# Performance work log

Measured on AMD Instinct MI355X. Metric: run time of the kernel, lower is better.

The kernel has to match this reference:

```python
import jax, jax.numpy as jnp
import numpy as np

B, T, H = 256, 512, 256


def setup_inputs() -> dict:
    key = jax.random.key(0)
    ks = jax.random.split(key, 16)
    s_in, s_h = 1.0 / np.sqrt(1.0), 1.0 / np.sqrt(H)

    def u(k, shape, s):
        return jax.random.uniform(k, shape, jnp.float32, -s, s)

    return {
        "x": jax.random.normal(ks[0], (B, T), jnp.float32),
        # LSTMCell 1: input size 1
        "W_ih1": u(ks[1], (4 * H, 1), s_h), "b_ih1": u(ks[2], (4 * H,), s_h),
        "W_hh1": u(ks[3], (4 * H, H), s_h), "b_hh1": u(ks[4], (4 * H,), s_h),
        # LSTMCell 2: input size H
        "W_ih2": u(ks[5], (4 * H, H), s_h), "b_ih2": u(ks[6], (4 * H,), s_h),
        "W_hh2": u(ks[7], (4 * H, H), s_h), "b_hh2": u(ks[8], (4 * H,), s_h),
        # SelfAttention linears
        "Wa1": u(ks[9], (H, H), s_h), "ba1": u(ks[10], (H,), s_h),
        "Wa2": u(ks[11], (H, H), s_h), "ba2": u(ks[12], (H,), s_h),
        # output linear H -> 1
        "Wo": u(ks[13], (1, H), s_h), "bo": u(ks[14], (1,), s_h),
        "future": 0,
    }


def _lstm_cell(h, c, gates):
    i, f, g, o = jnp.split(gates, 4, axis=-1)
    i, f, o = jax.nn.sigmoid(i), jax.nn.sigmoid(f), jax.nn.sigmoid(o)
    g = jnp.tanh(g)
    c = f * c + i * g
    return o * jnp.tanh(c), c


def reference(x, W_ih1, b_ih1, W_hh1, b_hh1, W_ih2, b_ih2, W_hh2, b_hh2,
              Wa1, ba1, Wa2, ba2, Wo, bo, future):
    n, Tt = x.shape
    Hd = W_hh1.shape[1]

    def step_core(h1, c1, h2, c2, x_t):
        # x_t: [B, 1]
        g1 = x_t @ W_ih1.T + b_ih1 + h1 @ W_hh1.T + b_hh1
        h1, c1 = _lstm_cell(h1, c1, g1)
        g2 = h1 @ W_ih2.T + b_ih2 + h2 @ W_hh2.T + b_hh2
        h2, c2 = _lstm_cell(h2, c2, g2)
        # additive self-attention (dropout p=0 -> identity)
        attn = jax.nn.softmax(jnp.tanh(h2 @ Wa1.T + ba1) @ Wa2.T + ba2, axis=-1)
        out = (attn * h2) @ Wo.T + bo  # [B, 1]
        return h1, c1, h2, c2, out

    def step(carry, x_t):
        h1, c1, h2, c2, _ = carry
        h1, c1, h2, c2, out = step_core(h1, c1, h2, c2, x_t)
        return (h1, c1, h2, c2, out), out

    z = jnp.zeros((n, Hd), x.dtype)
    init = (z, z, z, z, jnp.zeros((n, 1), x.dtype))
    xs = x.T[:, :, None]  # [T, B, 1]
    carry, outs = jax.lax.scan(step, init, xs)

    if future > 0:
        def fstep(carry, _):
            h1, c1, h2, c2, out = carry
            h1, c1, h2, c2, out = step_core(h1, c1, h2, c2, out)
            return (h1, c1, h2, c2, out), out
        _, fouts = jax.lax.scan(fstep, carry, None, length=future)
        outs = jnp.concatenate([outs, fouts], axis=0)

    return outs[:, :, 0].T  # [B, T+future]
```

## Files before the change

kernel.cpp:

```cpp
#include <hip/hip_runtime.h>
#include <hip/hip_bf16.h>

#define HD   256
#define TT   512

typedef unsigned short u16;
typedef unsigned int   u32;
typedef unsigned long long u64;
typedef __attribute__((ext_vector_type(8))) short  short8;
typedef __attribute__((ext_vector_type(4))) float  f32x4;

__device__ __forceinline__ float bf2f(u16 v) { return __uint_as_float(((u32)v) << 16); }
__device__ __forceinline__ u16 f2bf(float f) {
    u32 u = __float_as_uint(f);
    u32 r = u + 0x7fffu + ((u >> 16) & 1u);
    return (u16)(r >> 16);
}
__device__ __forceinline__ float sigf(float x)  { return __builtin_amdgcn_rcpf(1.f + __expf(-x)); }
__device__ __forceinline__ float tanhf_(float x){ float e = __expf(-2.f * x);
                                                  return 2.f * __builtin_amdgcn_rcpf(1.f + e) - 1.f; }

__global__ void cvt_bf_kernel(const float* __restrict__ src, u16* __restrict__ dst, int n) {
    int idx = blockIdx.x * 256 + threadIdx.x;
    if (idx < n) dst[idx] = f2bf(src[idx]);
}

__global__ void bias_kernel(const float* __restrict__ a1, const float* __restrict__ b1,
                            const float* __restrict__ a2, const float* __restrict__ b2,
                            float* __restrict__ o1, float* __restrict__ o2) {
    int i = blockIdx.x * 256 + threadIdx.x;
    o1[i] = a1[i] + b1[i];
    o2[i] = a2[i] + b2[i];
}

__device__ __forceinline__ void load_bfrag(const float* __restrict__ W, int row, int kq, short8* bw) {
#pragma unroll
    for (int kk = 0; kk < 8; ++kk) {
        const float* p = W + row * 256 + kk * 32 + kq * 8;
        short8 s;
#pragma unroll
        for (int j = 0; j < 8; ++j) s[j] = (short)f2bf(p[j]);
        bw[kk] = s;
    }
}

__device__ __forceinline__ u64 aload64(const u64* p) {
    return __hip_atomic_load(p, __ATOMIC_RELAXED, __HIP_MEMORY_SCOPE_AGENT);
}
__device__ __forceinline__ void astore32(u32* p, u32 v) {
    __hip_atomic_store(p, v, __ATOMIC_RELAXED, __HIP_MEMORY_SCOPE_AGENT);
}

__device__ __forceinline__ void flag_wait(const u32* flags, int gb, u32 target) {
    if (threadIdx.x < 8) {
        const u32* slot = flags + (gb * 8 + (int)threadIdx.x) * 32;
        int sp = 0;
        while (__hip_atomic_load(slot, __ATOMIC_RELAXED, __HIP_MEMORY_SCOPE_AGENT) < target) {
            if (++sp > (1 << 24)) break;
        }
    }
    __syncthreads();
}

__device__ __forceinline__ void flag_post(u32* flags, int slotidx, u32 val) {
    __syncthreads();
    if (threadIdx.x == 0)
        __hip_atomic_store(flags + slotidx * 32, val, __ATOMIC_RELAXED, __HIP_MEMORY_SCOPE_AGENT);
}

__global__ __launch_bounds__(512) void lstm_persist(
    const float* __restrict__ x,
    const float* __restrict__ Wih1,
    const float* __restrict__ bias1,
    const float* __restrict__ bias2,
    const float* __restrict__ Whh1,
    const float* __restrict__ Wih2,
    const float* __restrict__ Whh2,
    u32* __restrict__ Hb1, u32* __restrict__ Hb2,
    u16* __restrict__ H2out, u32* flags)
{
    __shared__ __align__(16) u16 sh1hi[16 * 264], sh1lo[16 * 264];
    __shared__ __align__(16) u16 sh2hi[16 * 264], sh2lo[16 * 264];
    __shared__ float xs[TT * 16];
    __shared__ float gbuf1[4 * 16 * 36], gbuf2[4 * 16 * 36];
    __shared__ float wihs[128], b1s[128], b2s[128];

    const int tid = threadIdx.x;
    const int blk = blockIdx.x;
    const int gb = blk >> 3, hg = blk & 7;
    const int l = tid & 63, wv = tid >> 6;
    const int g = wv >> 1, hh = wv & 1;
    const int nloc = l & 15, kq = l >> 4;
    const int wrow = g * 256 + hg * 32 + hh * 16 + nloc;

    short8 bW1[8], bW2[8], bW3[8];
    load_bfrag(Whh1, wrow, kq, bW1);
    load_bfrag(Wih2, wrow, kq, bW2);
    load_bfrag(Whh2, wrow, kq, bW3);

    for (int idx = tid; idx < 16 * TT; idx += 512) {
        int b = idx >> 9, t = idx & 511;
        xs[t * 16 + b] = x[(gb * 16 + b) * TT + t];
    }
    if (tid < 128) {
        int rr = (tid >> 5) * 256 + hg * 32 + (tid & 31);
        wihs[tid] = Wih1[rr]; b1s[tid] = bias1[rr]; b2s[tid] = bias2[rr];
    }

    const int cb = tid >> 5, ci = tid & 31;
    const int bg = gb * 16 + cb, ig = hg * 32 + ci;
#pragma unroll
    for (int pp = 0; pp < 2; ++pp) {
        astore32(&Hb1[((pp * 256 + bg) << 8) + ig], 0u);
        astore32(&Hb2[((pp * 256 + bg) << 8) + ig], 0u);
    }
    float c1 = 0.f, c2 = 0.f;

    flag_post(flags, gb * 8 + hg, 1u);

    const int aoff = nloc * 264 + kq * 8;
    const int sb = tid >> 5, scol = (tid & 31) * 8;
    const int sbase = sb * 264 + scol;

    for (int k = 0; k <= TT; ++k) {
        flag_wait(flags, gb, (u32)(k + 1));

        const int rp = k & 1, wp = rp ^ 1;
        {
            const u32* p1 = Hb1 + ((rp * 256 + gb * 16 + sb) << 8) + scol;
            const u32* p2 = Hb2 + ((rp * 256 + gb * 16 + sb) << 8) + scol;
            u32 w1v[8], w2v[8];
#pragma unroll
            for (int j = 0; j < 4; ++j) {
                u64 t = aload64((const u64*)p1 + j);
                w1v[2 * j] = (u32)t; w1v[2 * j + 1] = (u32)(t >> 32);
            }
#pragma unroll
            for (int j = 0; j < 4; ++j) {
                u64 t = aload64((const u64*)p2 + j);
                w2v[2 * j] = (u32)t; w2v[2 * j + 1] = (u32)(t >> 32);
            }
            u32 h1h[4], h1l[4], h2h[4], h2l[4];
#pragma unroll
            for (int i = 0; i < 4; ++i) {
                u32 a = w1v[2 * i], b = w1v[2 * i + 1];
                h1h[i] = (a & 0xffffu) | (b << 16);
                h1l[i] = (a >> 16) | (b & 0xffff0000u);
                a = w2v[2 * i]; b = w2v[2 * i + 1];
                h2h[i] = (a & 0xffffu) | (b << 16);
                h2l[i] = (a >> 16) | (b & 0xffff0000u);
            }
            *(uint4*)(sh1hi + sbase) = *(uint4*)(h1h);
            *(uint4*)(sh1lo + sbase) = *(uint4*)(h1l);
            *(uint4*)(sh2hi + sbase) = *(uint4*)(h2h);
            *(uint4*)(sh2lo + sbase) = *(uint4*)(h2l);
        }
        __syncthreads();

        f32x4 acc1a = {0,0,0,0}, acc1b = {0,0,0,0};
        f32x4 acc2a = {0,0,0,0}, acc2b = {0,0,0,0};
#pragma unroll
        for (int kk = 0; kk < 8; ++kk) {
            short8 a1h = *(const short8*)(sh1hi + aoff + kk * 32);
            short8 a1l = *(const short8*)(sh1lo + aoff + kk * 32);
            if (k < TT) {
                acc1a = __builtin_amdgcn_mfma_f32_16x16x32_bf16(a1h, bW1[kk], acc1a, 0, 0, 0);
                acc1b = __builtin_amdgcn_mfma_f32_16x16x32_bf16(a1l, bW1[kk], acc1b, 0, 0, 0);
            }
            if (k > 0) {
                acc2a = __builtin_amdgcn_mfma_f32_16x16x32_bf16(a1h, bW2[kk], acc2a, 0, 0, 0);
                acc2b = __builtin_amdgcn_mfma_f32_16x16x32_bf16(a1l, bW2[kk], acc2b, 0, 0, 0);
                short8 a2h = *(const short8*)(sh2hi + aoff + kk * 32);
                short8 a2l = *(const short8*)(sh2lo + aoff + kk * 32);
                acc2a = __builtin_amdgcn_mfma_f32_16x16x32_bf16(a2h, bW3[kk], acc2a, 0, 0, 0);
                acc2b = __builtin_amdgcn_mfma_f32_16x16x32_bf16(a2l, bW3[kk], acc2b, 0, 0, 0);
            }
        }
#pragma unroll
        for (int r = 0; r < 4; ++r) {
            int m = (l >> 4) * 4 + r;
            gbuf1[(g * 16 + m) * 36 + hh * 16 + nloc] = acc1a[r] + acc1b[r];
            gbuf2[(g * 16 + m) * 36 + hh * 16 + nloc] = acc2a[r] + acc2b[r];
        }
        __syncthreads();

        u16 hi2 = 0;
        if (k < TT) {
            float xv = xs[k * 16 + cb];
            float g0 = gbuf1[(0 * 16 + cb) * 36 + ci] + xv * wihs[ci]      + b1s[ci];
            float g1 = gbuf1[(1 * 16 + cb) * 36 + ci] + xv * wihs[32 + ci] + b1s[32 + ci];
            float g2 = gbuf1[(2 * 16 + cb) * 36 + ci] + xv * wihs[64 + ci] + b1s[64 + ci];
            float g3 = gbuf1[(3 * 16 + cb) * 36 + ci] + xv * wihs[96 + ci] + b1s[96 + ci];
            float ii = sigf(g0), ff = sigf(g1), gg = tanhf_(g2), oo = sigf(g3);
            c1 = ff * c1 + ii * gg;
            float h = oo * tanhf_(c1);
            u16 hi = f2bf(h); u32 word = (u32)hi | ((u32)f2bf(h - bf2f(hi)) << 16);
            astore32(&Hb1[((wp * 256 + bg) << 8) + ig], word);
        }
        if (k > 0) {
            float g0 = gbuf2[(0 * 16 + cb) * 36 + ci] + b2s[ci];
            float g1 = gbuf2[(1 * 16 + cb) * 36 + ci] + b2s[32 + ci];
            float g2 = gbuf2[(2 * 16 + cb) * 36 + ci] + b2s[64 + ci];
            float g3 = gbuf2[(3 * 16 + cb) * 36 + ci] + b2s[96 + ci];
            float ii = sigf(g0), ff = sigf(g1), gg = tanhf_(g2), oo = sigf(g3);
            c2 = ff * c2 + ii * gg;
            float h = oo * tanhf_(c2);
            hi2 = f2bf(h); u32 word = (u32)hi2 | ((u32)f2bf(h - bf2f(hi2)) << 16);
            astore32(&Hb2[((wp * 256 + bg) << 8) + ig], word);
        }
        flag_post(flags, gb * 8 + hg, (u32)(k + 2));
        if (k > 0) H2out[(bg * TT + (k - 1)) * 256 + ig] = hi2;
    }
}

__global__ __launch_bounds__(256) void attn_fused(
    const u16*  __restrict__ Wa1b, const u16* __restrict__ Wa2b,
    const float* __restrict__ ba1, const float* __restrict__ ba2,
    const float* __restrict__ Wo,  const float* __restrict__ bo,
    const u16*  __restrict__ H2,   float* __restrict__ out)
{
    __shared__ __align__(16) u16 sA[64 * 264];
    __shared__ __align__(16) u16 sP[64 * 264];
    __shared__ float red[64 * 12];
    __shared__ float sb1[256], sb2[256], swo[256];

    const int tid = threadIdx.x;
    const int w = tid >> 6, l = tid & 63;
    const int c = l & 15, q = l >> 4;
    const int row0 = blockIdx.x * 64;

    {
        const int r = tid >> 2, qq = tid & 3;
        const uint4* src = (const uint4*)(H2 + (row0 + r) * 256 + qq * 64);
#pragma unroll
        for (int j = 0; j < 8; ++j) {
            uint4 v = src[j];
            *(uint4*)(sA + r * 264 + qq * 64 + j * 8) = v;
        }
    }
    if (tid < 256) { sb1[tid] = ba1[tid]; sb2[tid] = ba2[tid]; swo[tid] = Wo[tid]; }
    __syncthreads();

    f32x4 acc[4][4];
#pragma unroll
    for (int mi = 0; mi < 4; ++mi)
#pragma unroll
        for (int ni = 0; ni < 4; ++ni) acc[mi][ni] = (f32x4){0,0,0,0};

#pragma unroll
    for (int ni = 0; ni < 4; ++ni) {
        const int row = w * 64 + ni * 16 + c;
        const u16* wp = Wa1b + row * 256 + q * 8;
        short8 bW[8];
#pragma unroll
        for (int kk = 0; kk < 8; ++kk) bW[kk] = *(const short8*)(wp + kk * 32);
#pragma unroll
        for (int kk = 0; kk < 8; ++kk)
#pragma unroll
            for (int mi = 0; mi < 4; ++mi) {
                short8 a = *(const short8*)(sA + (mi * 16 + c) * 264 + q * 8 + kk * 32);
                acc[mi][ni] = __builtin_amdgcn_mfma_f32_16x16x32_bf16(a, bW[kk], acc[mi][ni], 0, 0, 0);
            }
    }
#pragma unroll
    for (int mi = 0; mi < 4; ++mi)
#pragma unroll
        for (int ni = 0; ni < 4; ++ni) {
            const int n = w * 64 + ni * 16 + c;
            const float bj = sb1[n];
#pragma unroll
            for (int r = 0; r < 4; ++r) {
                int m = mi * 16 + q * 4 + r;
                sP[m * 264 + n] = f2bf(tanhf(acc[mi][ni][r] + bj));
            }
        }
    __syncthreads();

#pragma unroll
    for (int mi = 0; mi < 4; ++mi)
#pragma unroll
        for (int ni = 0; ni < 4; ++ni) acc[mi][ni] = (f32x4){0,0,0,0};
#pragma unroll
    for (int ni = 0; ni < 4; ++ni) {
        const int row = w * 64 + ni * 16 + c;
        const u16* wp = Wa2b + row * 256 + q * 8;
        short8 bW[8];
#pragma unroll
        for (int kk = 0; kk < 8; ++kk) bW[kk] = *(const short8*)(wp + kk * 32);
#pragma unroll
        for (int kk = 0; kk < 8; ++kk)
#pragma unroll
            for (int mi = 0; mi < 4; ++mi) {
                short8 a = *(const short8*)(sP + (mi * 16 + c) * 264 + q * 8 + kk * 32);
                acc[mi][ni] = __builtin_amdgcn_mfma_f32_16x16x32_bf16(a, bW[kk], acc[mi][ni], 0, 0, 0);
            }
    }

    float mx[4][4];
#pragma unroll
    for (int mi = 0; mi < 4; ++mi)
#pragma unroll
        for (int r = 0; r < 4; ++r) mx[mi][r] = -1e30f;
#pragma unroll
    for (int mi = 0; mi < 4; ++mi)
#pragma unroll
        for (int ni = 0; ni < 4; ++ni) {
            const float bj = sb2[w * 64 + ni * 16 + c];
#pragma unroll
            for (int r = 0; r < 4; ++r) {
                float s = acc[mi][ni][r] + bj;
                acc[mi][ni][r] = s;
                mx[mi][r] = fmaxf(mx[mi][r], s);
            }
        }
#pragma unroll
    for (int off = 1; off < 16; off <<= 1)
#pragma unroll
        for (int mi = 0; mi < 4; ++mi)
#pragma unroll
            for (int r = 0; r < 4; ++r) mx[mi][r] = fmaxf(mx[mi][r], __shfl_xor(mx[mi][r], off));
    if (c == 0)
#pragma unroll
        for (int mi = 0; mi < 4; ++mi)
#pragma unroll
            for (int r = 0; r < 4; ++r) red[(mi * 16 + q * 4 + r) * 12 + w] = mx[mi][r];
    __syncthreads();
#pragma unroll
    for (int mi = 0; mi < 4; ++mi)
#pragma unroll
        for (int r = 0; r < 4; ++r) {
            const float* rp = red + (mi * 16 + q * 4 + r) * 12;
            mx[mi][r] = fmaxf(fmaxf(rp[0], rp[1]), fmaxf(rp[2], rp[3]));
        }
    float suml[4][4], sumw[4][4];
#pragma unroll
    for (int mi = 0; mi < 4; ++mi)
#pragma unroll
        for (int r = 0; r < 4; ++r) { suml[mi][r] = 0.f; sumw[mi][r] = 0.f; }
#pragma unroll
    for (int mi = 0; mi < 4; ++mi)
#pragma unroll
        for (int ni = 0; ni < 4; ++ni) {
            const int n = w * 64 + ni * 16 + c;
            const float wov = swo[n];
#pragma unroll
            for (int r = 0; r < 4; ++r) {
                int m = mi * 16 + q * 4 + r;
                float e = __expf(acc[mi][ni][r] - mx[mi][r]);
                suml[mi][r] += e;
                sumw[mi][r] += e * bf2f(sA[m * 264 + n]) * wov;
            }
        }
#pragma unroll
    for (int off = 1; off < 16; off <<= 1)
#pragma unroll
        for (int mi = 0; mi < 4; ++mi)
#pragma unroll
            for (int r = 0; r < 4; ++r) {
                suml[mi][r] += __shfl_xor(suml[mi][r], off);
                sumw[mi][r] += __shfl_xor(sumw[mi][r], off);
            }
    __syncthreads();
    if (c == 0)
#pragma unroll
        for (int mi = 0; mi < 4; ++mi)
#pragma unroll
            for (int r = 0; r < 4; ++r) {
                int m = mi * 16 + q * 4 + r;
                red[m * 12 + 4 + w] = suml[mi][r];
                red[m * 12 + 8 + w] = sumw[mi][r];
            }
    __syncthreads();
    if (tid < 64) {
        const float* rp = red + tid * 12;
        float lsum = rp[4] + rp[5] + rp[6] + rp[7];
        float wsum = rp[8] + rp[9] + rp[10] + rp[11];
        out[row0 + tid] = wsum / lsum + bo[0];
    }
}

extern "C" void kernel_launch(void* const* d_in, const int* in_sizes, int n_in,
                              void* d_out, int out_size, void* d_ws, size_t ws_size,
                              hipStream_t stream) {
    const float* x    = (const float*)d_in[0];
    const float* Wih1 = (const float*)d_in[1];
    const float* bih1 = (const float*)d_in[2];
    const float* Whh1 = (const float*)d_in[3];
    const float* bhh1 = (const float*)d_in[4];
    const float* Wih2 = (const float*)d_in[5];
    const float* bih2 = (const float*)d_in[6];
    const float* Whh2 = (const float*)d_in[7];
    const float* bhh2 = (const float*)d_in[8];
    const float* Wa1  = (const float*)d_in[9];
    const float* ba1  = (const float*)d_in[10];
    const float* Wa2  = (const float*)d_in[11];
    const float* ba2  = (const float*)d_in[12];
    const float* Wo   = (const float*)d_in[13];
    const float* bo   = (const float*)d_in[14];

    char* ws = (char*)d_ws;
    u16*   Wa1b  = (u16*)(ws + 0);
    u16*   Wa2b  = (u16*)(ws + 131072);
    float* bias1 = (float*)(ws + 262144);
    float* bias2 = (float*)(ws + 266240);
    u32*   flags = (u32*)(ws + 270336);
    u32*   Hb1   = (u32*)(ws + 524288);
    u32*   Hb2   = (u32*)(ws + 1048576);
    u16*   H2    = (u16*)(ws + 2097152);
    float* out   = (float*)d_out;

    (void)hipMemsetAsync(flags, 0, 16384, stream);
    bias_kernel<<<4, 256, 0, stream>>>(bih1, bhh1, bih2, bhh2, bias1, bias2);
    cvt_bf_kernel<<<256, 256, 0, stream>>>(Wa1, Wa1b, 65536);
    cvt_bf_kernel<<<256, 256, 0, stream>>>(Wa2, Wa2b, 65536);

    lstm_persist<<<128, 512, 0, stream>>>(x, Wih1, bias1, bias2,
                                          Whh1, Wih2, Whh2, Hb1, Hb2, H2, flags);
    attn_fused<<<2048, 256, 0, stream>>>(Wa1b, Wa2b, ba1, ba2, Wo, bo, H2, out);
}
```

Measured before the change: 2.218 ms.

## Split layer flags and prefetch next-step hidden states when peers are ready

The single per-step flag is replaced by separate flags for the layer-1 and layer-2 hidden-state buffers. Each flag is posted as soon as its layer's hidden state is written, so peers can begin loading h1 before layer 2 finishes. At the end of each step the block polls all peer flags once and, if every peer is already done, loads the next step's hidden states early and skips the blocking wait. This aims to shorten the cross-block handoff latency on the serial recurrence, at the cost of extra barriers, an extra flag poll per step, and a smaller spin-timeout bound.

```diff
diff --git a/kernel.cpp b/kernel.cpp
--- a/kernel.cpp
+++ b/kernel.cpp
@@ -47,25 +47,21 @@
 __device__ __forceinline__ u64 aload64(const u64* p) {
     return __hip_atomic_load(p, __ATOMIC_RELAXED, __HIP_MEMORY_SCOPE_AGENT);
 }
+__device__ __forceinline__ u32 aload32(const u32* p) {
+    return __hip_atomic_load(p, __ATOMIC_RELAXED, __HIP_MEMORY_SCOPE_AGENT);
+}
 __device__ __forceinline__ void astore32(u32* p, u32 v) {
     __hip_atomic_store(p, v, __ATOMIC_RELAXED, __HIP_MEMORY_SCOPE_AGENT);
 }
 
-__device__ __forceinline__ void flag_wait(const u32* flags, int gb, u32 target) {
+__device__ __forceinline__ void flag_poll(const u32* flags, int gb, u32 target) {
     if (threadIdx.x < 8) {
         const u32* slot = flags + (gb * 8 + (int)threadIdx.x) * 32;
         int sp = 0;
-        while (__hip_atomic_load(slot, __ATOMIC_RELAXED, __HIP_MEMORY_SCOPE_AGENT) < target) {
-            if (++sp > (1 << 24)) break;
-        }
-    }
-    __syncthreads();
-}
-
-__device__ __forceinline__ void flag_post(u32* flags, int slotidx, u32 val) {
-    __syncthreads();
-    if (threadIdx.x == 0)
-        __hip_atomic_store(flags + slotidx * 32, val, __ATOMIC_RELAXED, __HIP_MEMORY_SCOPE_AGENT);
+        while (aload32(slot) < target) {
+            if (++sp > (1 << 20)) break;
+        }
+    }
 }
 
 __global__ __launch_bounds__(512) void lstm_persist(
@@ -77,13 +73,14 @@
     const float* __restrict__ Wih2,
     const float* __restrict__ Whh2,
     u32* __restrict__ Hb1, u32* __restrict__ Hb2,
-    u16* __restrict__ H2out, u32* flags)
+    u16* __restrict__ H2out, u32* flagsA, u32* flagsB)
 {
     __shared__ __align__(16) u16 sh1hi[16 * 264], sh1lo[16 * 264];
     __shared__ __align__(16) u16 sh2hi[16 * 264], sh2lo[16 * 264];
     __shared__ float xs[TT * 16];
     __shared__ float gbuf1[4 * 16 * 36], gbuf2[4 * 16 * 36];
     __shared__ float wihs[128], b1s[128], b2s[128];
+    __shared__ int s_pre;
 
     const int tid = threadIdx.x;
     const int blk = blockIdx.x;
@@ -116,29 +113,41 @@
     }
     float c1 = 0.f, c2 = 0.f;
 
-    flag_post(flags, gb * 8 + hg, 1u);
+    __syncthreads();
+    if (tid == 0) {
+        astore32(flagsA + (gb * 8 + hg) * 32, 1u);
+        astore32(flagsB + (gb * 8 + hg) * 32, 1u);
+    }
 
     const int aoff = nloc * 264 + kq * 8;
     const int sb = tid >> 5, scol = (tid & 31) * 8;
     const int sbase = sb * 264 + scol;
 
+    u64 v1[4], v2[4];
+    bool pre = false;
+
     for (int k = 0; k <= TT; ++k) {
-        flag_wait(flags, gb, (u32)(k + 1));
-
         const int rp = k & 1, wp = rp ^ 1;
+        const u64* p1 = (const u64*)(Hb1 + ((rp * 256 + gb * 16 + sb) << 8) + scol);
+        const u64* p2 = (const u64*)(Hb2 + ((rp * 256 + gb * 16 + sb) << 8) + scol);
+
+        if (!pre) {
+            flag_poll(flagsA, gb, (u32)(k + 1));
+            __syncthreads();
+#pragma unroll
+            for (int j = 0; j < 4; ++j) v1[j] = aload64(p1 + j);
+            flag_poll(flagsB, gb, (u32)(k + 1));
+            __syncthreads();
+#pragma unroll
+            for (int j = 0; j < 4; ++j) v2[j] = aload64(p2 + j);
+        }
+
         {
-            const u32* p1 = Hb1 + ((rp * 256 + gb * 16 + sb) << 8) + scol;
-            const u32* p2 = Hb2 + ((rp * 256 + gb * 16 + sb) << 8) + scol;
             u32 w1v[8], w2v[8];
 #pragma unroll
             for (int j = 0; j < 4; ++j) {
-                u64 t = aload64((const u64*)p1 + j);
-                w1v[2 * j] = (u32)t; w1v[2 * j + 1] = (u32)(t >> 32);
-            }
-#pragma unroll
-            for (int j = 0; j < 4; ++j) {
-                u64 t = aload64((const u64*)p2 + j);
-                w2v[2 * j] = (u32)t; w2v[2 * j + 1] = (u32)(t >> 32);
+                w1v[2 * j] = (u32)v1[j]; w1v[2 * j + 1] = (u32)(v1[j] >> 32);
+                w2v[2 * j] = (u32)v2[j]; w2v[2 * j + 1] = (u32)(v2[j] >> 32);
             }
             u32 h1h[4], h1l[4], h2h[4], h2l[4];
 #pragma unroll
@@ -184,7 +193,6 @@
         }
         __syncthreads();
 
-        u16 hi2 = 0;
         if (k < TT) {
             float xv = xs[k * 16 + cb];
             float g0 = gbuf1[(0 * 16 + cb) * 36 + ci] + xv * wihs[ci]      + b1s[ci];
@@ -197,6 +205,10 @@
             u16 hi = f2bf(h); u32 word = (u32)hi | ((u32)f2bf(h - bf2f(hi)) << 16);
             astore32(&Hb1[((wp * 256 + bg) << 8) + ig], word);
         }
+        __syncthreads();
+        if (tid == 0) astore32(flagsA + (gb * 8 + hg) * 32, (u32)(k + 2));
+
+        u16 hi2 = 0;
         if (k > 0) {
             float g0 = gbuf2[(0 * 16 + cb) * 36 + ci] + b2s[ci];
             float g1 = gbuf2[(1 * 16 + cb) * 36 + ci] + b2s[32 + ci];
@@ -208,8 +220,34 @@
             hi2 = f2bf(h); u32 word = (u32)hi2 | ((u32)f2bf(h - bf2f(hi2)) << 16);
             astore32(&Hb2[((wp * 256 + bg) << 8) + ig], word);
         }
-        flag_post(flags, gb * 8 + hg, (u32)(k + 2));
+        __syncthreads();
+        if (tid == 0) astore32(flagsB + (gb * 8 + hg) * 32, (u32)(k + 2));
+
         if (k > 0) H2out[(bg * TT + (k - 1)) * 256 + ig] = hi2;
+
+        pre = false;
+        if (k < TT) {
+            u32 fv = 0;
+            if (tid < 16) {
+                const u32* f = (tid < 8) ? flagsA : flagsB;
+                fv = aload32(f + (gb * 8 + (tid & 7)) * 32);
+            }
+            if (wv == 0) {
+                u64 bal = __ballot(tid < 16 ? (fv >= (u32)(k + 2)) : true);
+                if (l == 0) s_pre = ((bal & 0xffffull) == 0xffffull) ? 1 : 0;
+            }
+            __syncthreads();
+            if (s_pre) {
+                const int rp2 = (k + 1) & 1;
+                const u64* q1 = (const u64*)(Hb1 + ((rp2 * 256 + gb * 16 + sb) << 8) + scol);
+                const u64* q2 = (const u64*)(Hb2 + ((rp2 * 256 + gb * 16 + sb) << 8) + scol);
+#pragma unroll
+                for (int j = 0; j < 4; ++j) v1[j] = aload64(q1 + j);
+#pragma unroll
+                for (int j = 0; j < 4; ++j) v2[j] = aload64(q2 + j);
+                pre = true;
+            }
+        }
     }
 }
 
@@ -403,18 +441,19 @@
     u16*   Wa2b  = (u16*)(ws + 131072);
     float* bias1 = (float*)(ws + 262144);
     float* bias2 = (float*)(ws + 266240);
-    u32*   flags = (u32*)(ws + 270336);
+    u32*   flagsA= (u32*)(ws + 270336);
+    u32*   flagsB= (u32*)(ws + 286720);
     u32*   Hb1   = (u32*)(ws + 524288);
     u32*   Hb2   = (u32*)(ws + 1048576);
     u16*   H2    = (u16*)(ws + 2097152);
     float* out   = (float*)d_out;
 
-    (void)hipMemsetAsync(flags, 0, 16384, stream);
+    (void)hipMemsetAsync(ws + 270336, 0, 32768, stream);
     bias_kernel<<<4, 256, 0, stream>>>(bih1, bhh1, bih2, bhh2, bias1, bias2);
     cvt_bf_kernel<<<256, 256, 0, stream>>>(Wa1, Wa1b, 65536);
     cvt_bf_kernel<<<256, 256, 0, stream>>>(Wa2, Wa2b, 65536);
 
     lstm_persist<<<128, 512, 0, stream>>>(x, Wih1, bias1, bias2,
-                                          Whh1, Wih2, Whh2, Hb1, Hb2, H2, flags);
+                                          Whh1, Wih2, Whh2, Hb1, Hb2, H2, flagsA, flagsB);
     attn_fused<<<2048, 256, 0, stream>>>(Wa1b, Wa2b, ba1, ba2, Wo, bo, H2, out);
 }
```

New measurement: 2.235 ms. No clear change (+0.7%).
